# Optimization experiments

Measured on AMD Instinct MI355X. Metric: run time of the kernel, lower is better.

## Reference

```python
import jax, jax.numpy as jnp
import numpy as np

N = 50000          # num nodes
E = 800000         # num edges
IN_C, HID_C, OUT_C = 128, 256, 256
LN_EPS = 1e-5


def gcn_conv(x, W, b, row, col):
    """PyG GCNConv: h = D^{-1/2}(A+I)D^{-1/2} (x W) + b, self-loops added."""
    h = x @ W                                             # [N, C_out]
    deg = jax.ops.segment_sum(jnp.ones((row.shape[0],), h.dtype), col,
                              num_segments=N) + 1.0        # +1 for self-loop
    dinv = jax.lax.rsqrt(deg)                              # [N]
    msg = h[row] * (dinv[row] * dinv[col])[:, None]        # [E, C_out] gathered msgs
    agg = jax.ops.segment_sum(msg, col, num_segments=N)
    agg = agg + h * (dinv * dinv)[:, None]                 # self-loop contribution
    return agg + b


def layer_norm(x, gamma, beta):
    mu = jnp.mean(x, axis=-1, keepdims=True)
    var = jnp.mean(jnp.square(x - mu), axis=-1, keepdims=True)
    return (x - mu) * jax.lax.rsqrt(var + LN_EPS) * gamma + beta


def setup_inputs() -> dict:
    key = jax.random.key(0)
    ks = jax.random.split(key, 8)
    x = jax.random.normal(ks[0], (N, IN_C), jnp.float32)
    edge_index = jax.random.randint(ks[1], (2, E), 0, N, dtype=jnp.int64)
    W1 = jax.random.normal(ks[2], (IN_C, HID_C), jnp.float32) * (1.0 / np.sqrt(IN_C))
    b1 = jnp.zeros((HID_C,), jnp.float32)
    W2 = jax.random.normal(ks[3], (HID_C, OUT_C), jnp.float32) * (1.0 / np.sqrt(HID_C))
    b2 = jnp.zeros((OUT_C,), jnp.float32)
    ln1_g = jnp.ones((HID_C,), jnp.float32); ln1_b = jnp.zeros((HID_C,), jnp.float32)
    ln2_g = jnp.ones((OUT_C,), jnp.float32); ln2_b = jnp.zeros((OUT_C,), jnp.float32)
    proj_W = jax.random.normal(ks[4], (IN_C, OUT_C), jnp.float32) * (1.0 / np.sqrt(IN_C))
    proj_b = jnp.zeros((OUT_C,), jnp.float32)
    return {"x": x, "edge_index": edge_index, "W1": W1, "b1": b1, "W2": W2,
            "b2": b2, "ln1_g": ln1_g, "ln1_b": ln1_b, "ln2_g": ln2_g,
            "ln2_b": ln2_b, "proj_W": proj_W, "proj_b": proj_b}


def reference(x, edge_index, W1, b1, W2, b2, ln1_g, ln1_b, ln2_g, ln2_b,
              proj_W, proj_b):
    row, col = edge_index[0], edge_index[1]   # messages flow row -> col
    identity = x @ proj_W + proj_b            # self.proj (Linear, in != out)
    h = gcn_conv(x, W1, b1, row, col)
    h = jax.nn.relu(layer_norm(h, ln1_g, ln1_b))   # dropout = identity (eval)
    g = gcn_conv(h, W2, b2, row, col)
    g = layer_norm(g, ln2_g, ln2_b)
    return jax.nn.relu(g + identity)
```

## Files before the change

### kernel.cpp

```cpp
#include <hip/hip_runtime.h>

#define NN 50000
#define NE 800000
#define LN_EPS 1e-5f

using bf16x8 = __attribute__((ext_vector_type(8))) short;
using f32x4  = __attribute__((ext_vector_type(4))) float;

__device__ __forceinline__ float b2f(unsigned short u) {
    union { unsigned int i; float f; } c;
    c.i = ((unsigned int)u) << 16;
    return c.f;
}
__device__ __forceinline__ unsigned short f2b(float f) {
    union { float f; unsigned int i; } c;
    c.f = f;
    const unsigned int i = c.i;
    return (unsigned short)((i + 0x7FFFu + ((i >> 16) & 1u)) >> 16);
}

template <int ITERS>
__device__ __forceinline__ void stage_async(const short* __restrict__ g,
                                            short* __restrict__ l) {
    const int lane = threadIdx.x & 63;
    const int wv = threadIdx.x >> 6;
#pragma unroll
    for (int i = 0; i < ITERS; ++i) {
        const int u = i * 256 + wv * 64;
        __builtin_amdgcn_global_load_lds(
            (const __attribute__((address_space(1))) void*)(g + (size_t)(u + lane) * 8),
            (__attribute__((address_space(3))) void*)(l + (size_t)u * 8),
            16, 0, 0);
    }
}

template <int K>
__device__ __forceinline__ void pack_body(const float* __restrict__ W,
                                          short* __restrict__ Wp, int i) {
    constexpr int KB = K / 32;
    const int j = i & 7;
    const int l = (i >> 3) & 63;
    const int t = i >> 9;
    const int kb = t % KB;
    const int nt = t / KB;
    const int k = 32 * kb + 8 * (l >> 4) + j;
    const int n = 16 * nt + (l & 15);
    Wp[i] = (short)f2b(W[(size_t)k * 256 + n]);
}

__global__ __launch_bounds__(256) void prep_k(
    const float* __restrict__ x, const float* __restrict__ W1,
    const float* __restrict__ W2, const float* __restrict__ pW,
    short* __restrict__ xb, short* __restrict__ Wp1,
    short* __restrict__ Wp2, short* __restrict__ Wpp) {
    const int b = blockIdx.x;
    if (b < 6250) {
        const int i = b * 256 + threadIdx.x;
        const float4 v = ((const float4*)x)[i];
        ushort4 o;
        o.x = f2b(v.x); o.y = f2b(v.y); o.z = f2b(v.z); o.w = f2b(v.w);
        ((ushort4*)xb)[i] = o;
    } else if (b < 6250 + 128) {
        pack_body<128>(W1, Wp1, (b - 6250) * 256 + threadIdx.x);
    } else if (b < 6250 + 384) {
        pack_body<256>(W2, Wp2, (b - 6378) * 256 + threadIdx.x);
    } else {
        pack_body<128>(pW, Wpp, (b - 6634) * 256 + threadIdx.x);
    }
}

__global__ __launch_bounds__(256) void count_k(const int* __restrict__ col,
                                               int* __restrict__ rowptr) {
    const int e = blockIdx.x * 256 + threadIdx.x;
    if (e < NE) atomicAdd(&rowptr[col[e] + 1], 1);
}

__global__ __launch_bounds__(256) void block_sum_k(const int* __restrict__ p,
                                                   int* __restrict__ psum, int n) {
    __shared__ int sh[256];
    const int t = threadIdx.x;
    const int i = blockIdx.x * 256 + t;
    sh[t] = (i < n) ? p[i] : 0;
    __syncthreads();
#pragma unroll
    for (int off = 128; off > 0; off >>= 1) {
        if (t < off) sh[t] += sh[t + off];
        __syncthreads();
    }
    if (t == 0) psum[blockIdx.x] = sh[0];
}

__global__ __launch_bounds__(256) void scan_apply_k(int* __restrict__ p,
                                                    const int* __restrict__ psum,
                                                    float* __restrict__ dinv,
                                                    int n, int nblk) {
    __shared__ int sh[256];
    const int t = threadIdx.x;
    const int b = blockIdx.x;
    const int i = b * 256 + t;
    sh[t] = (t < b && t < nblk) ? psum[t] : 0;
    __syncthreads();
#pragma unroll
    for (int off = 128; off > 0; off >>= 1) {
        if (t < off) sh[t] += sh[t + off];
        __syncthreads();
    }
    const int carry = sh[0];
    __syncthreads();
    const int raw = (i < n) ? p[i] : 0;
    if (i >= 1 && i < n) dinv[i - 1] = rsqrtf((float)raw + 1.0f);
    sh[t] = raw;
    __syncthreads();
#pragma unroll
    for (int off = 1; off < 256; off <<= 1) {
        const int u = (t >= off) ? sh[t - off] : 0;
        __syncthreads();
        sh[t] += u;
        __syncthreads();
    }
    if (i < n) p[i] = sh[t] + carry;
}

__global__ __launch_bounds__(256) void fill_k(const int* __restrict__ row,
                                              const int* __restrict__ col,
                                              const float* __restrict__ dinv,
                                              int* __restrict__ rowptr,
                                              int2* __restrict__ pairs) {
    const int e = blockIdx.x * 256 + threadIdx.x;
    if (e >= NE) return;
    const int rr = row[e];
    const int pos = atomicAdd(&rowptr[col[e]], 1);
    int2 pr;
    pr.x = rr;
    pr.y = __float_as_int(dinv[rr]);
    pairs[pos] = pr;
}

__global__ __launch_bounds__(256) void gather1_k(const short* __restrict__ X,
                                                 const int* __restrict__ endptr,
                                                 const int2* __restrict__ pairs,
                                                 const float* __restrict__ dinv,
                                                 short* __restrict__ A1) {
    const int node = blockIdx.x * 4 + (threadIdx.x >> 6);
    const int lane = threadIdx.x & 63;
    if (node >= NN) return;
    const int start = node ? endptr[node - 1] : 0;
    const int end = endptr[node];

    float a0 = 0.f, a1 = 0.f;
    int j = start;
    for (; j + 3 < end; j += 4) {
        const int2 p0 = pairs[j], p1 = pairs[j + 1];
        const int2 p2 = pairs[j + 2], p3 = pairs[j + 3];
        const float w0 = __int_as_float(p0.y), w1 = __int_as_float(p1.y);
        const float w2 = __int_as_float(p2.y), w3 = __int_as_float(p3.y);
        const ushort2 v0 = ((const ushort2*)(X + (size_t)p0.x * 128))[lane];
        const ushort2 v1 = ((const ushort2*)(X + (size_t)p1.x * 128))[lane];
        const ushort2 v2 = ((const ushort2*)(X + (size_t)p2.x * 128))[lane];
        const ushort2 v3 = ((const ushort2*)(X + (size_t)p3.x * 128))[lane];
        a0 += b2f(v0.x) * w0 + b2f(v1.x) * w1 + b2f(v2.x) * w2 + b2f(v3.x) * w3;
        a1 += b2f(v0.y) * w0 + b2f(v1.y) * w1 + b2f(v2.y) * w2 + b2f(v3.y) * w3;
    }
    for (; j < end; ++j) {
        const int2 p0 = pairs[j];
        const float w0 = __int_as_float(p0.y);
        const ushort2 v0 = ((const ushort2*)(X + (size_t)p0.x * 128))[lane];
        a0 += b2f(v0.x) * w0;
        a1 += b2f(v0.y) * w0;
    }
    const float dc = dinv[node];
    const ushort2 h = ((const ushort2*)(X + (size_t)node * 128))[lane];
    a0 = (a0 + b2f(h.x) * dc) * dc;
    a1 = (a1 + b2f(h.y) * dc) * dc;
    ushort2 o;
    o.x = f2b(a0); o.y = f2b(a1);
    ((ushort2*)A1)[(size_t)node * 64 + lane] = o;
}

__global__ __launch_bounds__(256) void gather2_k(const short* __restrict__ H,
                                                 const int* __restrict__ endptr,
                                                 const int2* __restrict__ pairs,
                                                 const float* __restrict__ dinv,
                                                 short* __restrict__ agg) {
    const int node = blockIdx.x * 4 + (threadIdx.x >> 6);
    const int lane = threadIdx.x & 63;
    if (node >= NN) return;
    const int start = node ? endptr[node - 1] : 0;
    const int end = endptr[node];

    float a0 = 0.f, a1 = 0.f, a2 = 0.f, a3 = 0.f;
    int j = start;
    for (; j + 3 < end; j += 4) {
        const int2 p0 = pairs[j], p1 = pairs[j + 1];
        const int2 p2 = pairs[j + 2], p3 = pairs[j + 3];
        const float w0 = __int_as_float(p0.y), w1 = __int_as_float(p1.y);
        const float w2 = __int_as_float(p2.y), w3 = __int_as_float(p3.y);
        const ushort4 v0 = ((const ushort4*)(H + (size_t)p0.x * 256))[lane];
        const ushort4 v1 = ((const ushort4*)(H + (size_t)p1.x * 256))[lane];
        const ushort4 v2 = ((const ushort4*)(H + (size_t)p2.x * 256))[lane];
        const ushort4 v3 = ((const ushort4*)(H + (size_t)p3.x * 256))[lane];
        a0 += b2f(v0.x) * w0 + b2f(v1.x) * w1 + b2f(v2.x) * w2 + b2f(v3.x) * w3;
        a1 += b2f(v0.y) * w0 + b2f(v1.y) * w1 + b2f(v2.y) * w2 + b2f(v3.y) * w3;
        a2 += b2f(v0.z) * w0 + b2f(v1.z) * w1 + b2f(v2.z) * w2 + b2f(v3.z) * w3;
        a3 += b2f(v0.w) * w0 + b2f(v1.w) * w1 + b2f(v2.w) * w2 + b2f(v3.w) * w3;
    }
    for (; j < end; ++j) {
        const int2 p0 = pairs[j];
        const float w0 = __int_as_float(p0.y);
        const ushort4 v0 = ((const ushort4*)(H + (size_t)p0.x * 256))[lane];
        a0 += b2f(v0.x) * w0;
        a1 += b2f(v0.y) * w0;
        a2 += b2f(v0.z) * w0;
        a3 += b2f(v0.w) * w0;
    }
    const float dc = dinv[node];
    const ushort4 h = ((const ushort4*)(H + (size_t)node * 256))[lane];
    ushort4 o;
    o.x = f2b((a0 + b2f(h.x) * dc) * dc);
    o.y = f2b((a1 + b2f(h.y) * dc) * dc);
    o.z = f2b((a2 + b2f(h.z) * dc) * dc);
    o.w = f2b((a3 + b2f(h.w) * dc) * dc);
    ((ushort4*)agg)[(size_t)node * 64 + lane] = o;
}

template <int K, bool PROJ, bool OUT_BF16>
__global__ __launch_bounds__(256) void gemm_ln_k(
    const short* __restrict__ X, const short* __restrict__ Wp,
    const float* __restrict__ bias, const float* __restrict__ gamma,
    const float* __restrict__ beta, const short* __restrict__ Xp,
    const short* __restrict__ Wpp, const float* __restrict__ pbias,
    void* __restrict__ Yv) {
    constexpr int KB = K / 32;
    constexpr int CHUNK = 2048 * KB;
    __shared__ short lds[2][CHUNK];
    const int lane = threadIdx.x & 63;
    const int wv = threadIdx.x >> 6;
    const int row0 = blockIdx.x * 64 + wv * 16;
    const int r = row0 + (lane & 15);
    const int rc = (r < NN) ? r : (NN - 1);
    const int kof = 8 * (lane >> 4);
    const int colbase = lane & 15;

    bf16x8 a[KB];
#pragma unroll
    for (int kb = 0; kb < KB; ++kb)
        a[kb] = *(const bf16x8*)(X + (size_t)rc * K + 32 * kb + kof);
    bf16x8 ap[4];
    if (PROJ) {
#pragma unroll
        for (int kb = 0; kb < 4; ++kb)
            ap[kb] = *(const bf16x8*)(Xp + (size_t)rc * 128 + 32 * kb + kof);
    }

    stage_async<KB>(Wp, lds[0]);

    f32x4 acc[16];
#pragma unroll
    for (int c = 0; c < 4; ++c) {
        __syncthreads();
        if (c < 3)
            stage_async<KB>(Wp + (size_t)(c + 1) * CHUNK, lds[(c + 1) & 1]);
        else if (PROJ)
            stage_async<4>(Wpp, lds[0]);
        const short* buf = lds[c & 1];
#pragma unroll
        for (int ntl = 0; ntl < 4; ++ntl) {
            f32x4 cacc = {0.f, 0.f, 0.f, 0.f};
#pragma unroll
            for (int kb = 0; kb < KB; ++kb) {
                const bf16x8 b = ((const bf16x8*)buf)[(ntl * KB + kb) * 64 + lane];
                cacc = __builtin_amdgcn_mfma_f32_16x16x32_bf16(a[kb], b, cacc, 0, 0, 0);
            }
            acc[c * 4 + ntl] = cacc;
        }
    }

    float s[4] = {0.f, 0.f, 0.f, 0.f};
    float q[4] = {0.f, 0.f, 0.f, 0.f};
#pragma unroll
    for (int nt = 0; nt < 16; ++nt) {
        const float bv = bias[nt * 16 + colbase];
#pragma unroll
        for (int rg = 0; rg < 4; ++rg) {
            const float v = acc[nt][rg] + bv;
            acc[nt][rg] = v;
            s[rg] += v;
            q[rg] += v * v;
        }
    }
#pragma unroll
    for (int off = 1; off < 16; off <<= 1) {
#pragma unroll
        for (int rg = 0; rg < 4; ++rg) {
            s[rg] += __shfl_xor(s[rg], off, 64);
            q[rg] += __shfl_xor(q[rg], off, 64);
        }
    }
    float mu[4], rsd[4];
#pragma unroll
    for (int rg = 0; rg < 4; ++rg) {
        mu[rg] = s[rg] * (1.f / 256.f);
        const float var = q[rg] * (1.f / 256.f) - mu[rg] * mu[rg];
        rsd[rg] = rsqrtf(var + LN_EPS);
    }

    const int orow0 = row0 + (lane >> 4) * 4;
    if (PROJ) {
#pragma unroll
        for (int pc = 0; pc < 4; ++pc) {
            __syncthreads();
            if (pc < 3)
                stage_async<4>(Wpp + (size_t)(pc + 1) * 8192, lds[(pc + 1) & 1]);
            const short* buf = lds[pc & 1];
#pragma unroll
            for (int ntl = 0; ntl < 4; ++ntl) {
                const int nt = pc * 4 + ntl;
                f32x4 pid = {0.f, 0.f, 0.f, 0.f};
#pragma unroll
                for (int kb = 0; kb < 4; ++kb) {
                    const bf16x8 b = ((const bf16x8*)buf)[(ntl * 4 + kb) * 64 + lane];
                    pid = __builtin_amdgcn_mfma_f32_16x16x32_bf16(ap[kb], b, pid, 0, 0, 0);
                }
                const int col = nt * 16 + colbase;
                const float g = gamma[col];
                const float be = beta[col];
                const float pbv = pbias[col];
#pragma unroll
                for (int rg = 0; rg < 4; ++rg) {
                    const int orow = orow0 + rg;
                    float v = (acc[nt][rg] - mu[rg]) * rsd[rg] * g + be;
                    v += pid[rg] + pbv;
                    v = fmaxf(v, 0.f);
                    if (orow < NN) {
                        if (OUT_BF16)
                            ((short*)Yv)[(size_t)orow * 256 + col] = (short)f2b(v);
                        else
                            ((float*)Yv)[(size_t)orow * 256 + col] = v;
                    }
                }
            }
        }
    } else {
#pragma unroll
        for (int nt = 0; nt < 16; ++nt) {
            const int col = nt * 16 + colbase;
            const float g = gamma[col];
            const float be = beta[col];
#pragma unroll
            for (int rg = 0; rg < 4; ++rg) {
                const int orow = orow0 + rg;
                float v = (acc[nt][rg] - mu[rg]) * rsd[rg] * g + be;
                v = fmaxf(v, 0.f);
                if (orow < NN) {
                    if (OUT_BF16)
                        ((short*)Yv)[(size_t)orow * 256 + col] = (short)f2b(v);
                    else
                        ((float*)Yv)[(size_t)orow * 256 + col] = v;
                }
            }
        }
    }
}

extern "C" void kernel_launch(void* const* d_in, const int* in_sizes, int n_in,
                              void* d_out, int out_size, void* d_ws, size_t ws_size,
                              hipStream_t stream) {
    const float* x    = (const float*)d_in[0];
    const int*   eidx = (const int*)d_in[1];
    const float* W1   = (const float*)d_in[2];
    const float* b1   = (const float*)d_in[3];
    const float* W2   = (const float*)d_in[4];
    const float* b2   = (const float*)d_in[5];
    const float* ln1g = (const float*)d_in[6];
    const float* ln1b = (const float*)d_in[7];
    const float* ln2g = (const float*)d_in[8];
    const float* ln2b = (const float*)d_in[9];
    const float* pW   = (const float*)d_in[10];
    const float* pb   = (const float*)d_in[11];

    const int* row = eidx;
    const int* col = eidx + NE;
    float* out = (float*)d_out;

    short* xb     = (short*)d_ws;
    short* A1     = xb + (size_t)NN * 128;
    short* Bb     = A1 + (size_t)NN * 128;
    short* Ag     = Bb + (size_t)NN * 256;
    float* dinv   = (float*)(Ag + (size_t)NN * 256);
    int*   rowptr = (int*)(dinv + NN);
    int*   psum   = rowptr + NN + 4;
    int2*  pairs  = (int2*)(psum + 256);
    short* Wp1    = (short*)(pairs + NE);
    short* Wp2    = Wp1 + 128 * 256;
    short* Wpp    = Wp2 + 256 * 256;

    const int nscan = NN + 1;
    const int nblk = (nscan + 255) / 256;

    hipMemsetAsync(rowptr, 0, (NN + 4) * sizeof(int), stream);
    prep_k<<<6762, 256, 0, stream>>>(x, W1, W2, pW, xb, Wp1, Wp2, Wpp);
    count_k<<<(NE + 255) / 256, 256, 0, stream>>>(col, rowptr);
    block_sum_k<<<nblk, 256, 0, stream>>>(rowptr, psum, nscan);
    scan_apply_k<<<nblk, 256, 0, stream>>>(rowptr, psum, dinv, nscan, nblk);
    fill_k<<<(NE + 255) / 256, 256, 0, stream>>>(row, col, dinv, rowptr, pairs);

    gather1_k<<<(NN + 3) / 4, 256, 0, stream>>>(xb, rowptr, pairs, dinv, A1);
    gemm_ln_k<128, false, true><<<(NN + 63) / 64, 256, 0, stream>>>(
        A1, Wp1, b1, ln1g, ln1b, nullptr, nullptr, nullptr, Bb);

    gather2_k<<<(NN + 3) / 4, 256, 0, stream>>>(Bb, rowptr, pairs, dinv, Ag);
    gemm_ln_k<256, true, false><<<(NN + 63) / 64, 256, 0, stream>>>(
        Ag, Wp2, b2, ln2g, ln2b, xb, Wpp, pb, out);
}
```

Measured before the change: 278.3 us.

## Unroll gather loops by eight and use fixed-size LDS chunks in GEMM-LN

The gather kernels now batch eight edge-pair loads, then eight row loads, before accumulating. This raises memory-level parallelism in the latency-bound neighbour gathers. The GEMM kernel now stages weights in fixed 8192-element LDS chunks, so K=256 runs eight phases of two column tiles each instead of four large phases. This cuts LDS use and may improve occupancy, at the cost of more barriers. The projection weights now go into the alternate buffer rather than always buffer 0.

```diff
diff --git a/kernel.cpp b/kernel.cpp
--- a/kernel.cpp
+++ b/kernel.cpp
@@ -149,17 +149,20 @@
 
     float a0 = 0.f, a1 = 0.f;
     int j = start;
-    for (; j + 3 < end; j += 4) {
-        const int2 p0 = pairs[j], p1 = pairs[j + 1];
-        const int2 p2 = pairs[j + 2], p3 = pairs[j + 3];
-        const float w0 = __int_as_float(p0.y), w1 = __int_as_float(p1.y);
-        const float w2 = __int_as_float(p2.y), w3 = __int_as_float(p3.y);
-        const ushort2 v0 = ((const ushort2*)(X + (size_t)p0.x * 128))[lane];
-        const ushort2 v1 = ((const ushort2*)(X + (size_t)p1.x * 128))[lane];
-        const ushort2 v2 = ((const ushort2*)(X + (size_t)p2.x * 128))[lane];
-        const ushort2 v3 = ((const ushort2*)(X + (size_t)p3.x * 128))[lane];
-        a0 += b2f(v0.x) * w0 + b2f(v1.x) * w1 + b2f(v2.x) * w2 + b2f(v3.x) * w3;
-        a1 += b2f(v0.y) * w0 + b2f(v1.y) * w1 + b2f(v2.y) * w2 + b2f(v3.y) * w3;
+    for (; j + 7 < end; j += 8) {
+        int2 p[8];
+        ushort2 v[8];
+#pragma unroll
+        for (int u = 0; u < 8; ++u) p[u] = pairs[j + u];
+#pragma unroll
+        for (int u = 0; u < 8; ++u)
+            v[u] = ((const ushort2*)(X + (size_t)p[u].x * 128))[lane];
+#pragma unroll
+        for (int u = 0; u < 8; ++u) {
+            const float w = __int_as_float(p[u].y);
+            a0 += b2f(v[u].x) * w;
+            a1 += b2f(v[u].y) * w;
+        }
     }
     for (; j < end; ++j) {
         const int2 p0 = pairs[j];
@@ -190,19 +193,22 @@
 
     float a0 = 0.f, a1 = 0.f, a2 = 0.f, a3 = 0.f;
     int j = start;
-    for (; j + 3 < end; j += 4) {
-        const int2 p0 = pairs[j], p1 = pairs[j + 1];
-        const int2 p2 = pairs[j + 2], p3 = pairs[j + 3];
-        const float w0 = __int_as_float(p0.y), w1 = __int_as_float(p1.y);
-        const float w2 = __int_as_float(p2.y), w3 = __int_as_float(p3.y);
-        const ushort4 v0 = ((const ushort4*)(H + (size_t)p0.x * 256))[lane];
-        const ushort4 v1 = ((const ushort4*)(H + (size_t)p1.x * 256))[lane];
-        const ushort4 v2 = ((const ushort4*)(H + (size_t)p2.x * 256))[lane];
-        const ushort4 v3 = ((const ushort4*)(H + (size_t)p3.x * 256))[lane];
-        a0 += b2f(v0.x) * w0 + b2f(v1.x) * w1 + b2f(v2.x) * w2 + b2f(v3.x) * w3;
-        a1 += b2f(v0.y) * w0 + b2f(v1.y) * w1 + b2f(v2.y) * w2 + b2f(v3.y) * w3;
-        a2 += b2f(v0.z) * w0 + b2f(v1.z) * w1 + b2f(v2.z) * w2 + b2f(v3.z) * w3;
-        a3 += b2f(v0.w) * w0 + b2f(v1.w) * w1 + b2f(v2.w) * w2 + b2f(v3.w) * w3;
+    for (; j + 7 < end; j += 8) {
+        int2 p[8];
+        ushort4 v[8];
+#pragma unroll
+        for (int u = 0; u < 8; ++u) p[u] = pairs[j + u];
+#pragma unroll
+        for (int u = 0; u < 8; ++u)
+            v[u] = ((const ushort4*)(H + (size_t)p[u].x * 256))[lane];
+#pragma unroll
+        for (int u = 0; u < 8; ++u) {
+            const float w = __int_as_float(p[u].y);
+            a0 += b2f(v[u].x) * w;
+            a1 += b2f(v[u].y) * w;
+            a2 += b2f(v[u].z) * w;
+            a3 += b2f(v[u].w) * w;
+        }
     }
     for (; j < end; ++j) {
         const int2 p0 = pairs[j];
@@ -231,7 +237,9 @@
     const short* __restrict__ Wpp, const float* __restrict__ pbias,
     void* __restrict__ Yv) {
     constexpr int KB = K / 32;
-    constexpr int CHUNK = 2048 * KB;
+    constexpr int NTC = 16 / KB;
+    constexpr int NPH = 16 / NTC;
+    constexpr int CHUNK = 8192;
     __shared__ short lds[2][CHUNK];
     const int lane = threadIdx.x & 63;
     const int wv = threadIdx.x >> 6;
@@ -252,26 +260,26 @@
             ap[kb] = *(const bf16x8*)(Xp + (size_t)rc * 128 + 32 * kb + kof);
     }
 
-    stage_async<KB>(Wp, lds[0]);
+    stage_async<4>(Wp, lds[0]);
 
     f32x4 acc[16];
 #pragma unroll
-    for (int c = 0; c < 4; ++c) {
+    for (int c = 0; c < NPH; ++c) {
         __syncthreads();
-        if (c < 3)
-            stage_async<KB>(Wp + (size_t)(c + 1) * CHUNK, lds[(c + 1) & 1]);
+        if (c < NPH - 1)
+            stage_async<4>(Wp + (size_t)(c + 1) * CHUNK, lds[(c + 1) & 1]);
         else if (PROJ)
-            stage_async<4>(Wpp, lds[0]);
+            stage_async<4>(Wpp, lds[(c + 1) & 1]);
         const short* buf = lds[c & 1];
 #pragma unroll
-        for (int ntl = 0; ntl < 4; ++ntl) {
+        for (int ntl = 0; ntl < NTC; ++ntl) {
             f32x4 cacc = {0.f, 0.f, 0.f, 0.f};
 #pragma unroll
             for (int kb = 0; kb < KB; ++kb) {
                 const bf16x8 b = ((const bf16x8*)buf)[(ntl * KB + kb) * 64 + lane];
                 cacc = __builtin_amdgcn_mfma_f32_16x16x32_bf16(a[kb], b, cacc, 0, 0, 0);
             }
-            acc[c * 4 + ntl] = cacc;
+            acc[c * NTC + ntl] = cacc;
         }
     }
 
```

Result: no change. 277.3 us, median of 2 (-0.3%).
